# Kernel optimization log

Hardware: AMD Instinct MI355X
Metric: run time of the kernel (lower is better)

The kernel has to match this reference:

```python
import jax, jax.numpy as jnp
import numpy as np
from jax import lax

C, H, W_ = 256, 384, 384

def setup_inputs() -> dict:
    key = jax.random.key(0)
    k1, k2, k3, k4 = jax.random.split(key, 4)
    return {
        'input1': jax.random.normal(k1, (1, C, H, W_), dtype=jnp.float32),
        'input2': jax.random.normal(k2, (1, C, H, W_), dtype=jnp.float32),
        'W': jax.random.normal(k3, (C, C, 3, 3), dtype=jnp.float32) * (1.0 / np.sqrt(C * 9)),
        'b': jax.random.normal(k4, (C,), dtype=jnp.float32) * 0.01,
    }

def _conv(x, W, b):
    # nn.Conv2d(C, C, 3, stride=1, padding=0)
    y = lax.conv_general_dilated(x, W, window_strides=(1, 1), padding='VALID',
                                 dimension_numbers=('NCHW', 'OIHW', 'NCHW'))
    return y + b[None, :, None, None]

def _ca(x):
    # adaptive_avg_pool2d to (1,1) then sigmoid -> [1, C, 1, 1]
    return jax.nn.sigmoid(jnp.mean(x, axis=(2, 3), keepdims=True))

def reference(input1, input2, W, b):
    input3 = input1 + input2
    x1 = _ca(_conv(input1, W, b))
    x2 = _ca(_conv(input2, W, b))
    x3 = _ca(_conv(input3, W, b))
    # Vectorized replication of the per-channel branch logic (ties: x1==x2 fires both blocks)
    c1 = x1 >= x2
    c2 = x1 <= x2
    dt = input1.dtype
    adj1 = (c1 & (x1 >= x3)).astype(dt)
    adj2 = (c2 & (x2 >= x3)).astype(dt)
    adj3 = ((c1 & (x1 < x3)) | (c2 & (x2 < x3))).astype(dt)
    return adj1 * input1 + adj2 * input2 + adj3 * input3
```

## Files before the change

### kernel.cpp

```cpp
#include <hip/hip_runtime.h>


#define CH 256
#define WD 384
#define ROW_F4 96
#define CH_F4 (WD * WD / 4)
#define CH_ELEMS (WD * WD)

__device__ inline double wave_reduce(double v) {
    #pragma unroll
    for (int off = 32; off > 0; off >>= 1)
        v += __shfl_down(v, off, 64);
    return v;
}

__global__ __launch_bounds__(256) void sums_kernel(
    const float* __restrict__ in1, const float* __restrict__ in2,
    double* __restrict__ S )
{
    int bid = blockIdx.x;
    int inp = bid >> 8;
    int c   = bid & 255;
    const float* base = (inp ? in2 : in1) + (size_t)c * CH_ELEMS;
    const float4* p = (const float4*)base;
    int tid = threadIdx.x;

    double T = 0, C0 = 0, C1 = 0, C382 = 0, C383 = 0;
    double R0 = 0, R1 = 0, R382 = 0, R383 = 0;

    for (int i = tid; i < CH_F4; i += 256) {
        float4 v = p[i];
        int r  = i / ROW_F4;
        int c4 = i - r * ROW_F4;
        double s = ((double)v.x + (double)v.y) + ((double)v.z + (double)v.w);
        T += s;
        if (c4 == 0)          { C0   += (double)v.x; C1   += (double)v.y; }
        if (c4 == ROW_F4 - 1) { C382 += (double)v.z; C383 += (double)v.w; }
        if      (r == 0)      R0   += s;
        else if (r == 1)      R1   += s;
        else if (r == WD - 2) R382 += s;
        else if (r == WD - 1) R383 += s;
    }

    __shared__ double red[4][9];
    double vals[9] = {T, C0, C1, C382, C383, R0, R1, R382, R383};
    int lane = tid & 63, wv = tid >> 6;
    #pragma unroll
    for (int k = 0; k < 9; k++) {
        double r = wave_reduce(vals[k]);
        if (lane == 0) red[wv][k] = r;
    }
    __syncthreads();

    if (tid == 0) {
        double a[9];
        #pragma unroll
        for (int k = 0; k < 9; k++)
            a[k] = (red[0][k] + red[1][k]) + (red[2][k] + red[3][k]);
        double Tt = a[0], c0 = a[1], c1 = a[2], c382 = a[3], c383 = a[4];
        double r0 = a[5], r1 = a[6], r382 = a[7], r383 = a[8];

        double x00 = base[0*WD+0],   x01 = base[0*WD+1],   x0a = base[0*WD+382],   x0b = base[0*WD+383];
        double x10 = base[1*WD+0],   x11 = base[1*WD+1],   x1a = base[1*WD+382],   x1b = base[1*WD+383];
        double xa0 = base[382*WD+0], xa1 = base[382*WD+1], xaa = base[382*WD+382], xab = base[382*WD+383];
        double xb0 = base[383*WD+0], xb1 = base[383*WD+1], xba = base[383*WD+382], xbb = base[383*WD+383];

        double Tot[3] = { Tt - c382 - c383, Tt - c0 - c383, Tt - c0 - c1 };
        double rp0[3] = { r0 - x0a - x0b,   r0 - x00 - x0b,   r0 - x00 - x01 };
        double rp1[3] = { r1 - x1a - x1b,   r1 - x10 - x1b,   r1 - x10 - x11 };
        double rpa[3] = { r382 - xaa - xab, r382 - xa0 - xab, r382 - xa0 - xa1 };
        double rpb[3] = { r383 - xba - xbb, r383 - xb0 - xbb, r383 - xb0 - xb1 };

        double* out = S + ((size_t)inp * CH + c) * 9;
        #pragma unroll
        for (int kw = 0; kw < 3; kw++) {
            out[0*3 + kw] = Tot[kw] - rpa[kw] - rpb[kw];
            out[1*3 + kw] = Tot[kw] - rp0[kw] - rpb[kw];
            out[2*3 + kw] = Tot[kw] - rp0[kw] - rp1[kw];
        }
    }
}

__global__ __launch_bounds__(256) void coef_kernel(
    const float* __restrict__ Wt, const float* __restrict__ b,
    const double* __restrict__ S, float* __restrict__ K )
{
    int co = blockIdx.x;
    int tid = threadIdx.x;
    const float*  wrow = Wt + (size_t)co * 2304;
    const double* S1 = S;
    const double* S2 = S + 2304;
    double y1 = 0, y2 = 0;
    for (int j = tid; j < 2304; j += 256) {
        double w = (double)wrow[j];
        y1 += w * S1[j];
        y2 += w * S2[j];
    }
    __shared__ double red[4][2];
    int lane = tid & 63, wv = tid >> 6;
    y1 = wave_reduce(y1);
    y2 = wave_reduce(y2);
    if (lane == 0) { red[wv][0] = y1; red[wv][1] = y2; }
    __syncthreads();
    if (tid == 0) {
        double Y1 = (red[0][0] + red[1][0]) + (red[2][0] + red[3][0]);
        double Y2 = (red[0][1] + red[1][1]) + (red[2][1] + red[3][1]);
        const double inv = 1.0 / 145924.0;
        double bb = (double)b[co];
        double m1 = bb + Y1 * inv;
        double m2 = bb + Y2 * inv;
        double m3 = bb + (Y1 + Y2) * inv;
        bool c1 = (m1 >= m2), c2 = (m1 <= m2);
        float adj1 = (c1 && m1 >= m3) ? 1.0f : 0.0f;
        float adj2 = (c2 && m2 >= m3) ? 1.0f : 0.0f;
        float adj3 = ((c1 && m1 < m3) || (c2 && m2 < m3)) ? 1.0f : 0.0f;
        K[2*co]     = adj1 + adj3;
        K[2*co + 1] = adj2 + adj3;
    }
}

__global__ __launch_bounds__(256) void mix_kernel(
    const float* __restrict__ in1, const float* __restrict__ in2,
    const float* __restrict__ K, float* __restrict__ out)
{
    int c = blockIdx.y;
    size_t idx = (size_t)c * CH_F4 + (size_t)blockIdx.x * 256 + threadIdx.x;
    const float4* a4 = (const float4*)in1;
    const float4* b4 = (const float4*)in2;
    float4* o4 = (float4*)out;
    float k1 = K[2*c], k2 = K[2*c + 1];
    float4 a = a4[idx], bv = b4[idx];
    float4 o;
    o.x = k1*a.x + k2*bv.x;
    o.y = k1*a.y + k2*bv.y;
    o.z = k1*a.z + k2*bv.z;
    o.w = k1*a.w + k2*bv.w;
    o4[idx] = o;
}

extern "C" void kernel_launch(void* const* d_in, const int* in_sizes, int n_in,
                              void* d_out, int out_size, void* d_ws, size_t ws_size,
                              hipStream_t stream) {
    const float* in1 = (const float*)d_in[0];
    const float* in2 = (const float*)d_in[1];
    const float* Wt  = (const float*)d_in[2];
    const float* b   = (const float*)d_in[3];
    float* out = (float*)d_out;

    double* S = (double*)d_ws;
    float*  K = (float*)((char*)d_ws + 2 * CH * 9 * sizeof(double));

    sums_kernel<<<512, 256, 0, stream>>>(in1, in2, S);
    coef_kernel<<<CH, 256, 0, stream>>>(Wt, b, S, K);
    mix_kernel<<<dim3(CH_F4 / 256, CH), 256, 0, stream>>>(in1, in2, K, out);
}
```

Before: 437.3 us.

## Split per-channel sums into chunked blocks and streamline mix kernel stores

The channel-sum pass now uses four blocks per channel, each covering 96 rows with a fully unrolled load loop. Border column and row sums are read directly by a few threads instead of being tested with per-element branches, and a second small kernel combines the chunk partials and applies the border corrections. The mix kernel now processes two float4s per thread and writes its output with nontemporal stores. The aim is more parallelism and memory-level concurrency in the reduction, less index arithmetic, and less cache pollution from the output, at the cost of one extra kernel launch.

```diff
diff --git a/kernel.cpp b/kernel.cpp
--- a/kernel.cpp
+++ b/kernel.cpp
@@ -6,6 +6,11 @@
 #define ROW_F4 96
 #define CH_F4 (WD * WD / 4)
 #define CH_ELEMS (WD * WD)
+#define NCHUNK 4
+#define CHUNK_ROWS 96
+#define CHUNK_F4 (CHUNK_ROWS * ROW_F4)
+
+typedef float v4f __attribute__((ext_vector_type(4)));
 
 __device__ inline double wave_reduce(double v) {
     #pragma unroll
@@ -14,32 +19,44 @@
     return v;
 }
 
-__global__ __launch_bounds__(256) void sums_kernel(
+__global__ __launch_bounds__(256) void sumsA_kernel(
     const float* __restrict__ in1, const float* __restrict__ in2,
-    double* __restrict__ S )
+    double* __restrict__ P )
 {
-    int bid = blockIdx.x;
-    int inp = bid >> 8;
-    int c   = bid & 255;
-    const float* base = (inp ? in2 : in1) + (size_t)c * CH_ELEMS;
-    const float4* p = (const float4*)base;
+    int bid   = blockIdx.x;
+    int chunk = bid & 3;
+    int c     = (bid >> 2) & 255;
+    int inp   = bid >> 10;
+    const float4* p = (const float4*)((inp ? in2 : in1) + (size_t)c * CH_ELEMS)
+                      + (size_t)chunk * CHUNK_F4;
     int tid = threadIdx.x;
 
-    double T = 0, C0 = 0, C1 = 0, C382 = 0, C383 = 0;
+    double T0 = 0, T1 = 0;
+    #pragma unroll
+    for (int k = 0; k < 36; k += 2) {
+        float4 v0 = p[tid + k * 256];
+        float4 v1 = p[tid + (k + 1) * 256];
+        T0 += ((double)v0.x + (double)v0.y) + ((double)v0.z + (double)v0.w);
+        T1 += ((double)v1.x + (double)v1.y) + ((double)v1.z + (double)v1.w);
+    }
+    double T = T0 + T1;
+
+    double C0 = 0, C1 = 0, C382 = 0, C383 = 0;
+    if (tid < CHUNK_ROWS) {
+        float4 a = p[tid * ROW_F4];
+        float4 z = p[tid * ROW_F4 + ROW_F4 - 1];
+        C0 = a.x; C1 = a.y; C382 = z.z; C383 = z.w;
+    }
     double R0 = 0, R1 = 0, R382 = 0, R383 = 0;
-
-    for (int i = tid; i < CH_F4; i += 256) {
-        float4 v = p[i];
-        int r  = i / ROW_F4;
-        int c4 = i - r * ROW_F4;
+    if (chunk == 0 && tid < 2 * ROW_F4) {
+        float4 v = p[tid];
         double s = ((double)v.x + (double)v.y) + ((double)v.z + (double)v.w);
-        T += s;
-        if (c4 == 0)          { C0   += (double)v.x; C1   += (double)v.y; }
-        if (c4 == ROW_F4 - 1) { C382 += (double)v.z; C383 += (double)v.w; }
-        if      (r == 0)      R0   += s;
-        else if (r == 1)      R1   += s;
-        else if (r == WD - 2) R382 += s;
-        else if (r == WD - 1) R383 += s;
+        if (tid < ROW_F4) R0 = s; else R1 = s;
+    }
+    if (chunk == 3 && tid < 2 * ROW_F4) {
+        float4 v = p[CHUNK_F4 - 2 * ROW_F4 + tid];
+        double s = ((double)v.x + (double)v.y) + ((double)v.z + (double)v.w);
+        if (tid < ROW_F4) R382 = s; else R383 = s;
     }
 
     __shared__ double red[4][9];
@@ -51,12 +68,27 @@
         if (lane == 0) red[wv][k] = r;
     }
     __syncthreads();
+    if (tid < 9) {
+        P[(size_t)bid * 9 + tid] =
+            (red[0][tid] + red[1][tid]) + (red[2][tid] + red[3][tid]);
+    }
+}
 
+__global__ __launch_bounds__(64) void sumsB_kernel(
+    const float* __restrict__ in1, const float* __restrict__ in2,
+    const double* __restrict__ P, double* __restrict__ S )
+{
+    int b = blockIdx.x;
+    int inp = b >> 8, c = b & 255;
+    int tid = threadIdx.x;
+    __shared__ double a[9];
+    if (tid < 9) {
+        const double* pp = P + (size_t)b * 36 + tid;
+        a[tid] = (pp[0] + pp[9]) + (pp[18] + pp[27]);
+    }
+    __syncthreads();
     if (tid == 0) {
-        double a[9];
-        #pragma unroll
-        for (int k = 0; k < 9; k++)
-            a[k] = (red[0][k] + red[1][k]) + (red[2][k] + red[3][k]);
+        const float* base = (inp ? in2 : in1) + (size_t)c * CH_ELEMS;
         double Tt = a[0], c0 = a[1], c1 = a[2], c382 = a[3], c383 = a[4];
         double r0 = a[5], r1 = a[6], r382 = a[7], r383 = a[8];
 
@@ -71,7 +103,7 @@
         double rpa[3] = { r382 - xaa - xab, r382 - xa0 - xab, r382 - xa0 - xa1 };
         double rpb[3] = { r383 - xba - xbb, r383 - xb0 - xbb, r383 - xb0 - xb1 };
 
-        double* out = S + ((size_t)inp * CH + c) * 9;
+        double* out = S + (size_t)b * 9;
         #pragma unroll
         for (int kw = 0; kw < 3; kw++) {
             out[0*3 + kw] = Tot[kw] - rpa[kw] - rpb[kw];
@@ -124,18 +156,20 @@
     const float* __restrict__ K, float* __restrict__ out)
 {
     int c = blockIdx.y;
-    size_t idx = (size_t)c * CH_F4 + (size_t)blockIdx.x * 256 + threadIdx.x;
+    size_t idx = (size_t)c * CH_F4 + (size_t)blockIdx.x * 512 + threadIdx.x;
     const float4* a4 = (const float4*)in1;
     const float4* b4 = (const float4*)in2;
-    float4* o4 = (float4*)out;
+    v4f* o4 = (v4f*)out;
     float k1 = K[2*c], k2 = K[2*c + 1];
-    float4 a = a4[idx], bv = b4[idx];
-    float4 o;
-    o.x = k1*a.x + k2*bv.x;
-    o.y = k1*a.y + k2*bv.y;
-    o.z = k1*a.z + k2*bv.z;
-    o.w = k1*a.w + k2*bv.w;
-    o4[idx] = o;
+    float4 a0 = a4[idx],       b0 = b4[idx];
+    float4 a1 = a4[idx + 256], b1 = b4[idx + 256];
+    v4f o0, o1;
+    o0.x = k1*a0.x + k2*b0.x; o0.y = k1*a0.y + k2*b0.y;
+    o0.z = k1*a0.z + k2*b0.z; o0.w = k1*a0.w + k2*b0.w;
+    o1.x = k1*a1.x + k2*b1.x; o1.y = k1*a1.y + k2*b1.y;
+    o1.z = k1*a1.z + k2*b1.z; o1.w = k1*a1.w + k2*b1.w;
+    __builtin_nontemporal_store(o0, &o4[idx]);
+    __builtin_nontemporal_store(o1, &o4[idx + 256]);
 }
 
 extern "C" void kernel_launch(void* const* d_in, const int* in_sizes, int n_in,
@@ -147,10 +181,12 @@
     const float* b   = (const float*)d_in[3];
     float* out = (float*)d_out;
 
-    double* S = (double*)d_ws;
-    float*  K = (float*)((char*)d_ws + 2 * CH * 9 * sizeof(double));
+    double* P = (double*)d_ws;
+    double* S = (double*)((char*)d_ws + 2 * CH * NCHUNK * 9 * sizeof(double));
+    float*  K = (float*)((char*)S + 2 * CH * 9 * sizeof(double));
 
-    sums_kernel<<<512, 256, 0, stream>>>(in1, in2, S);
+    sumsA_kernel<<<2 * CH * NCHUNK, 256, 0, stream>>>(in1, in2, P);
+    sumsB_kernel<<<2 * CH, 64, 0, stream>>>(in1, in2, P, S);
     coef_kernel<<<CH, 256, 0, stream>>>(Wt, b, S, K);
-    mix_kernel<<<dim3(CH_F4 / 256, CH), 256, 0, stream>>>(in1, in2, K, out);
+    mix_kernel<<<dim3(CH_F4 / 512, CH), 256, 0, stream>>>(in1, in2, K, out);
 }
```

New measurement: 405.0 us. 1.08x faster.
